# Kernel optimization log

Measured on AMD Instinct MI355X. Metric: run time of the kernel, lower is better.

Reference implementation:

```python
import jax, jax.numpy as jnp
import numpy as np

D_IN, D_HEAD, D_EXPAND, D_OUT, H = 512, 64, 2048, 512, 8
D_Q = D_HEAD * H  # 512
D_K = D_HEAD * H  # 512
D_V = D_IN * H    # 4096 (non-standard: per-head value dim = d_in)
EPS = 1e-5


def layernorm(x, g, b):
    mu = jnp.mean(x, axis=-1, keepdims=True)
    var = jnp.mean(jnp.square(x - mu), axis=-1, keepdims=True)
    return (x - mu) * jax.lax.rsqrt(var + EPS) * g + b


def setup_inputs() -> dict:
    key = jax.random.key(0)
    ks = jax.random.split(key, 12)
    B, N = 2, 2048
    s_in = 1.0 / np.sqrt(D_IN)
    s_mh = 1.0 / np.sqrt(D_IN * H)
    s_ex = 1.0 / np.sqrt(D_EXPAND)
    return {
        "x": jax.random.normal(ks[0], (B, N, D_IN), jnp.float32),
        "ln1_g": jnp.ones((D_IN,), jnp.float32),
        "ln1_b": jnp.zeros((D_IN,), jnp.float32),
        "Wqkv": jax.random.normal(ks[1], (D_IN, D_Q + D_K + D_V), jnp.float32) * s_in,
        "bqkv": jax.random.normal(ks[2], (D_Q + D_K + D_V,), jnp.float32) * 0.01,
        "Wm": jax.random.normal(ks[3], (D_IN * H, D_IN), jnp.float32) * s_mh,
        "bm": jax.random.normal(ks[4], (D_IN,), jnp.float32) * 0.01,
        "ln2_g": jnp.ones((D_IN,), jnp.float32),
        "ln2_b": jnp.zeros((D_IN,), jnp.float32),
        "W1": jax.random.normal(ks[5], (D_IN, D_EXPAND), jnp.float32) * s_in,
        "b1": jax.random.normal(ks[6], (D_EXPAND,), jnp.float32) * 0.01,
        "W2": jax.random.normal(ks[7], (D_EXPAND, D_OUT), jnp.float32) * s_ex,
        "b2": jax.random.normal(ks[8], (D_OUT,), jnp.float32) * 0.01,
    }


def reference(x, ln1_g, ln1_b, Wqkv, bqkv, Wm, bm, ln2_g, ln2_b, W1, b1, W2, b2):
    B, N, _ = x.shape
    scale = D_HEAD ** -0.5
    qkv = layernorm(x, ln1_g, ln1_b) @ Wqkv + bqkv
    q, k, v = jnp.split(qkv, [D_Q, D_Q + D_K], axis=-1)
    q = q.reshape(B, N, H, D_HEAD).transpose(0, 2, 1, 3)  # (B,H,N,dh)
    k = k.reshape(B, N, H, D_HEAD).transpose(0, 2, 1, 3)
    v = v.reshape(B, N, H, D_IN).transpose(0, 2, 1, 3)    # (B,H,N,d_in)
    attn = jax.nn.softmax(jnp.einsum('bhnd,bhmd->bhnm', q, k) * scale, axis=-1)
    out = jnp.einsum('bhnm,bhmc->bhnc', attn, v)          # (B,H,N,d_in)
    out = out.transpose(0, 2, 1, 3).reshape(B, N, H * D_IN)
    x2 = x + out @ Wm + bm
    h = layernorm(x2, ln2_g, ln2_b) @ W1 + b1
    h = h * jax.nn.sigmoid(h)  # Swish
    return h @ W2 + b2 + x2    # shortcut = Identity (d_in == d_out)
```

## Files before the change

kernel.cpp:

```cpp
#include <hip/hip_runtime.h>
#include <cmath>

typedef unsigned short u16;
typedef unsigned int   u32;
typedef __attribute__((ext_vector_type(8))) __bf16 bf16x8;
typedef __attribute__((ext_vector_type(4))) float  f32x4;
typedef __attribute__((ext_vector_type(8))) unsigned short u16x8;
typedef __attribute__((ext_vector_type(4))) unsigned short u16x4;

#define DEV __device__ __forceinline__

DEV float bf2f(u16 u){ union{u32 i; float f;} v; v.i=((u32)u)<<16; return v.f; }
DEV u16 f2bf(float f){ union{float f; u32 i;} v; v.f=f; u32 r=v.i+0x7fffu+((v.i>>16)&1u); return (u16)(r>>16); }

#if defined(__has_builtin) && __has_builtin(__builtin_amdgcn_global_load_lds)
DEV void gld16(const void* g, void* l){
  __builtin_amdgcn_global_load_lds((__attribute__((address_space(1))) void*)g,
                                   (__attribute__((address_space(3))) void*)l, 16, 0, 0);
}
#else
DEV void gld16(const void* g, void* l){ *(u16x8*)l = *(const u16x8*)g; }
#endif

#if defined(__has_builtin) && __has_builtin(__builtin_amdgcn_exp2f)
DEV float fexp2(float x){ return __builtin_amdgcn_exp2f(x); }
#else
DEV float fexp2(float x){ return exp2f(x); }
#endif

__global__ void detect_k(const u16* __restrict__ x, int* __restrict__ flag)
{
  if (threadIdx.x == 0 && blockIdx.x == 0){
    int sane = 0;
    for (int i = 0; i < 64; ++i){
      int e = (x[i] >> 7) & 0xFF;
      sane += (e >= 100 && e <= 150);
    }
    *flag = (sane < 56) ? 1 : 0;
  }
}

__global__ __launch_bounds__(256)
void conv_vecs(const void* a0,const void* a1,const void* a2,const void* a3,
               const void* a4,const void* a5,const void* a6,const void* a7,
               float* __restrict__ dst, const int* __restrict__ flag)
{
  int i = blockIdx.x*256 + threadIdx.x;
  if (i >= 10240) return;
  const void* src; int off;
  if      (i < 512)  { src=a0; off=i; }
  else if (i < 1024) { src=a1; off=i-512; }
  else if (i < 6144) { src=a2; off=i-1024; }
  else if (i < 6656) { src=a3; off=i-6144; }
  else if (i < 7168) { src=a4; off=i-6656; }
  else if (i < 7680) { src=a5; off=i-7168; }
  else if (i < 9728) { src=a6; off=i-7680; }
  else               { src=a7; off=i-9728; }
  dst[i] = (*flag) ? ((const float*)src)[off] : bf2f(((const u16*)src)[off]);
}

#define SWZ_SRC(c) (((c)&7) ^ (((c)>>3)&7))

template<int SWZ>
DEV void remap_xcd(int& bx, int& by)
{
  if (SWZ==1){
    int L = by*(int)gridDim.x + bx;
    int xcd = L & 7, l = L >> 3;
    int chunk = (int)gridDim.x >> 3;
    bx = xcd*chunk + (l % chunk);
    by = l / chunk;
  } else if (SWZ==2){
    int L = by*(int)gridDim.x + bx;
    int xcd = L & 7, l = L >> 3;
    int chunk = (int)gridDim.y >> 3;
    by = xcd*chunk + (l % chunk);
    bx = l / chunk;
  }
}

template<int MODE, int SWZ, bool VT>
__global__ __launch_bounds__(256)
void gemm_bt(const u16* __restrict__ A, const u16* __restrict__ BT,
             void* __restrict__ C, const float* __restrict__ bias,
             int K, int lda, int ldb, int ldc, u16* __restrict__ vout)
{
  __shared__ u16 AB[2*128*64];
  u16* As = AB;
  u16* Bs = AB + 128*64;
  const int tid  = threadIdx.x;
  const int lane = tid & 63;
  const int quad = lane>>4, l7 = lane&7, l15 = lane&15;
  const int wv   = tid >> 6;
  const int wm   = wv >> 1, wn = wv & 1;
  int bx = blockIdx.x, by = blockIdx.y;
  remap_xcd<SWZ>(bx, by);
  const long m0 = (long)by * 128;
  const long n0 = (long)bx * 128;

  f32x4 acc[4][4];
#pragma unroll
  for (int i=0;i<4;i++)
#pragma unroll
    for (int j=0;j<4;j++) acc[i][j] = (f32x4){0.f,0.f,0.f,0.f};

  for (int k0=0; k0<K; k0+=64){
    __syncthreads();
#pragma unroll
    for (int i=0;i<4;i++){
      int c = i*256 + tid;
      gld16(A  + (m0 + (c>>3))*lda + k0 + SWZ_SRC(c)*8, &As[c*8]);
      gld16(BT + (n0 + (c>>3))*ldb + k0 + SWZ_SRC(c)*8, &Bs[c*8]);
    }
    __syncthreads();
#pragma unroll
    for (int kk=0;kk<2;kk++){
      const int ch = ((kk*4 + quad) ^ l7) * 8;
      bf16x8 af[4], bfr[4];
#pragma unroll
      for (int t=0;t<4;t++){
        af[t]  = *(const bf16x8*)&As[(wm*64 + t*16 + l15)*64 + ch];
        bfr[t] = *(const bf16x8*)&Bs[(wn*64 + t*16 + l15)*64 + ch];
      }
#pragma unroll
      for (int ti=0;ti<4;ti++)
#pragma unroll
        for (int tj=0;tj<4;tj++)
          acc[ti][tj] = __builtin_amdgcn_mfma_f32_16x16x32_bf16(af[ti], bfr[tj], acc[ti][tj], 0,0,0);
    }
  }

  if (VT && n0 >= 1024){
    const int hh   = (int)((n0 - 1024) >> 9);
    const int c0   = (int)((n0 - 1024) & 511);
    const int b_   = (int)(m0 >> 11);
    const int kloc = (int)(m0 & 2047);
    u16* vb = vout + ((long)(b_*8 + hh))*512*2048 + kloc;
    u16* Ts = AB;
    __syncthreads();
#pragma unroll
    for (int pass=0; pass<2; ++pass){
      if (pass) __syncthreads();
      if (wn == pass){
#pragma unroll
        for (int ti=0;ti<4;ti++)
#pragma unroll
        for (int tj=0;tj<4;tj++)
#pragma unroll
        for (int r=0;r<4;r++){
          int row = wm*64 + ti*16 + quad*4 + r;
          int cl  = tj*16 + l15;
          float v = acc[ti][tj][r] + bias[n0 + pass*64 + cl];
          Ts[row*68 + cl] = f2bf(v);
        }
      }
      __syncthreads();
#pragma unroll
      for (int step=0; step<4; ++step){
        int cr = step*16 + (tid>>4);
        int t8 = (tid&15)*8;
        u16x8 pk;
#pragma unroll
        for (int j=0;j<8;j++) pk[j] = Ts[(t8+j)*68 + cr];
        *(u16x8*)(vb + (long)(c0 + pass*64 + cr)*2048 + t8) = pk;
      }
    }
    return;
  }

#pragma unroll
  for (int ti=0;ti<4;ti++)
#pragma unroll
  for (int tj=0;tj<4;tj++)
#pragma unroll
  for (int r=0;r<4;r++){
    long row = m0 + wm*64 + ti*16 + quad*4 + r;
    long col = n0 + wn*64 + tj*16 + l15;
    float v = acc[ti][tj][r] + bias[col];
    if (MODE==2) v = v / (1.f + __expf(-v));
    ((u16*)C)[row*ldc+col] = f2bf(v);
  }
}

template<int MODE, int SWZ>
__global__ __launch_bounds__(512)
void gemm_n64(const u16* __restrict__ A, const u16* __restrict__ BT,
              void* __restrict__ C, const float* __restrict__ bias,
              const void* __restrict__ res,
              int K, int lda, int ldb, int ldc, const int* __restrict__ flag)
{
  __shared__ u16 As[2][128*64];
  __shared__ u16 Bs[2][64*64];
  const int tid  = threadIdx.x;
  const int lane = tid & 63;
  const int quad = lane>>4, l7 = lane&7, l15 = lane&15;
  const int wm   = tid >> 6;
  int bx = blockIdx.x, by = blockIdx.y;
  remap_xcd<SWZ>(bx, by);
  const long m0 = (long)by * 128;
  const long n0 = (long)bx * 64;
  const bool f32io = flag && (*flag != 0);

  f32x4 acc[4];
#pragma unroll
  for (int j=0;j<4;j++) acc[j] = (f32x4){0.f,0.f,0.f,0.f};

  auto stage = [&](int bi, int k0){
#pragma unroll
    for (int i=0;i<2;i++){
      int c = i*512 + tid;
      gld16(A + (m0 + (c>>3))*lda + k0 + SWZ_SRC(c)*8, &As[bi][c*8]);
    }
    { int c = tid;
      gld16(BT + (n0 + (c>>3))*ldb + k0 + SWZ_SRC(c)*8, &Bs[bi][c*8]); }
  };

  const int S = K >> 6;
  stage(0, 0);
  __syncthreads();

  for (int s=0; s<S; ++s){
    const int cb = s & 1;
    if (s+1 < S) stage(cb^1, (s+1)<<6);
#pragma unroll
    for (int kk=0;kk<2;kk++){
      const int ch = ((kk*4 + quad) ^ l7) * 8;
      bf16x8 af = *(const bf16x8*)&As[cb][(wm*16 + l15)*64 + ch];
      bf16x8 bfr[4];
#pragma unroll
      for (int t=0;t<4;t++)
        bfr[t] = *(const bf16x8*)&Bs[cb][(t*16 + l15)*64 + ch];
#pragma unroll
      for (int tj=0;tj<4;tj++)
        acc[tj] = __builtin_amdgcn_mfma_f32_16x16x32_bf16(af, bfr[tj], acc[tj], 0,0,0);
    }
    __syncthreads();
  }

#pragma unroll
  for (int tj=0;tj<4;tj++)
#pragma unroll
  for (int r=0;r<4;r++){
    long row = m0 + wm*16 + quad*4 + r;
    long col = n0 + tj*16 + l15;
    float v = acc[tj][r] + bias[col];
    if (MODE==1){
      v += f32io ? ((const float*)res)[row*ldc+col]
                 : bf2f(((const u16*)res)[row*ldc+col]);
      ((float*)C)[row*ldc+col] = v;
    } else {
      v += ((const float*)res)[row*ldc+col];
      if (f32io) ((float*)C)[row*ldc+col] = v;
      else       ((u16*)C)[row*ldc+col]   = f2bf(v);
    }
  }
}

__global__ __launch_bounds__(512, 2)
void att_flash(const u16* __restrict__ qkv, const u16* __restrict__ vt,
               u16* __restrict__ ao)
{
  __shared__ u16 Qs[128*64];
  __shared__ u16 Ks[2][64*64];
  __shared__ u16 Ps[128*68];
  __shared__ u16 Vs[512*64];
  __shared__ float m_run[128], l_run[128], alph[128];
  __shared__ int resc[2];
  const int tid=threadIdx.x, lane=tid&63, wv=tid>>6;
  const int wm=wv>>2, wn=wv&3;
  const int quad=lane>>4, l7=lane&7, l15=lane&15;
  const int bid = blockIdx.x;
  const int id  = ((bid&7)<<5) + (bid>>3);
  const int qt  = id & 15, bh = id >> 4;
  const int b = bh>>3, h = bh&7;
  const long q0 = (long)qt*128;
  const u16* qb = qkv + ((long)b*2048 + q0)*5120 + h*64;
  const u16* kb = qkv + (long)b*2048*5120 + 512 + h*64;
  const u16* vb = vt + (long)bh*512*2048;

#pragma unroll
  for (int i=0;i<2;i++){
    int c=i*512+tid;
    gld16(qb + (long)(c>>3)*5120 + SWZ_SRC(c)*8, &Qs[c*8]);
  }
  { int c=tid; gld16(kb + (long)(c>>3)*5120 + SWZ_SRC(c)*8, &Ks[0][c*8]); }
  if (tid<128){ m_run[tid] = -1e30f; l_run[tid] = 0.f; }
  if (tid==0){ resc[0]=0; resc[1]=0; }

  f32x4 o[4][8];
#pragma unroll
  for (int i=0;i<4;i++)
#pragma unroll
    for (int j=0;j<8;j++) o[i][j] = (f32x4){0.f,0.f,0.f,0.f};

  __syncthreads();
  bf16x8 qreg[2];
#pragma unroll
  for (int kk=0;kk<2;kk++)
    qreg[kk] = *(const bf16x8*)&Qs[(wv*16 + l15)*64 + ((kk*4 + quad) ^ l7)*8];

  for (int mt=0; mt<32; ++mt){
    const long m0 = (long)mt*64;
    const int cur = mt&1;
    __syncthreads();

    if (mt < 31){ int c=tid; gld16(kb + (m0+64 + (c>>3))*5120 + SWZ_SRC(c)*8, &Ks[cur^1][c*8]); }
#pragma unroll
    for (int i=0;i<8;i++){
      int c=i*512+tid;
      gld16(vb + (long)(c>>3)*2048 + m0 + SWZ_SRC(c)*8, &Vs[c*8]);
    }
    if (tid==0) resc[cur^1] = 0;

    f32x4 s[4];
#pragma unroll
    for (int j=0;j<4;j++) s[j] = (f32x4){0.f,0.f,0.f,0.f};
#pragma unroll
    for (int kk=0;kk<2;kk++){
      const int ch = ((kk*4 + quad) ^ l7) * 8;
#pragma unroll
      for (int tj=0;tj<4;tj++){
        bf16x8 bfr = *(const bf16x8*)&Ks[cur][(tj*16 + l15)*64 + ch];
        s[tj] = __builtin_amdgcn_mfma_f32_16x16x32_bf16(qreg[kk], bfr, s[tj], 0,0,0);
      }
    }

    float nm[4], al[4], rs[4];
    bool chg = false;
#pragma unroll
    for (int r=0;r<4;r++){
      float vm = fmaxf(fmaxf(s[0][r],s[1][r]), fmaxf(s[2][r],s[3][r]));
      vm = fmaxf(vm, __shfl_xor(vm,1)); vm = fmaxf(vm, __shfl_xor(vm,2));
      vm = fmaxf(vm, __shfl_xor(vm,4)); vm = fmaxf(vm, __shfl_xor(vm,8));
      float mo = m_run[wv*16 + quad*4 + r];
      float vs = vm*0.125f;
      bool c_ = (vs > mo + 8.f);
      nm[r] = c_ ? vs : mo;
      al[r] = c_ ? __expf(mo - vs) : 1.f;
      chg |= c_;
      rs[r] = 0.f;
    }
    float nml[4];
#pragma unroll
    for (int r=0;r<4;r++) nml[r] = nm[r]*1.44269504f;
#pragma unroll
    for (int tj=0;tj<4;tj++)
#pragma unroll
    for (int r=0;r<4;r++){
      float pv = fexp2(fmaf(s[tj][r], 0.18033688f, -nml[r]));
      rs[r] += pv;
      Ps[(wv*16 + quad*4 + r)*68 + tj*16 + l15] = f2bf(pv);
    }
#pragma unroll
    for (int r=0;r<4;r++){
      rs[r] += __shfl_xor(rs[r],1); rs[r] += __shfl_xor(rs[r],2);
      rs[r] += __shfl_xor(rs[r],4); rs[r] += __shfl_xor(rs[r],8);
    }
    if (l15==0){
#pragma unroll
      for (int r=0;r<4;r++){
        int row = wv*16 + quad*4 + r;
        alph[row]  = al[r];
        m_run[row] = nm[r];
        l_run[row] = l_run[row]*al[r] + rs[r];
      }
    }
    if (__any((int)chg) && lane==0) resc[cur] = 1;
    __syncthreads();

    if (resc[cur]){
      float a_[4][4];
#pragma unroll
      for (int ti=0;ti<4;ti++)
#pragma unroll
        for (int r=0;r<4;r++) a_[ti][r] = alph[wm*64 + ti*16 + quad*4 + r];
#pragma unroll
      for (int ti=0;ti<4;ti++)
#pragma unroll
      for (int tj=0;tj<8;tj++)
#pragma unroll
        for (int r=0;r<4;r++) o[ti][tj][r] *= a_[ti][r];
    }
#pragma unroll
    for (int kk=0;kk<2;kk++){
      const int ch = ((kk*4 + quad) ^ l7) * 8;
      bf16x8 af[4], bfr[8];
#pragma unroll
      for (int t=0;t<4;t++){
        int base = (wm*64 + t*16 + l15)*68 + kk*32 + quad*8;
        union { u16x4 hh[2]; bf16x8 v; } u;
        u.hh[0] = *(const u16x4*)&Ps[base];
        u.hh[1] = *(const u16x4*)&Ps[base+4];
        af[t] = u.v;
      }
#pragma unroll
      for (int t=0;t<8;t++)
        bfr[t] = *(const bf16x8*)&Vs[(wn*128 + t*16 + l15)*64 + ch];
#pragma unroll
      for (int ti=0;ti<4;ti++)
#pragma unroll
        for (int tj=0;tj<8;tj++)
          o[ti][tj] = __builtin_amdgcn_mfma_f32_16x16x32_bf16(af[ti], bfr[tj], o[ti][tj], 0,0,0);
    }
  }

  float rl[4][4];
#pragma unroll
  for (int ti=0;ti<4;ti++)
#pragma unroll
    for (int r=0;r<4;r++) rl[ti][r] = 1.f / l_run[wm*64 + ti*16 + quad*4 + r];
#pragma unroll
  for (int ti=0;ti<4;ti++)
#pragma unroll
  for (int tj=0;tj<8;tj++)
#pragma unroll
  for (int r=0;r<4;r++){
    long rown = q0 + wm*64 + ti*16 + quad*4 + r;
    long col  = wn*128 + tj*16 + l15;
    ao[((long)b*2048 + rown)*4096 + (long)h*512 + col] = f2bf(o[ti][tj][r]*rl[ti][r]);
  }
}

template<int SRC>
__global__ __launch_bounds__(256)
void ln_kernel(const void* __restrict__ xin, const float* __restrict__ g,
               const float* __restrict__ bb, u16* __restrict__ out,
               const int* __restrict__ flag)
{
  const int tid=threadIdx.x, lane=tid&63, wv=tid>>6;
  const long row = (long)blockIdx.x*4 + wv;
  const bool f32 = (SRC==1) || (flag && *flag != 0);
  float v[8];
  if (f32){
    const float* xr = (const float*)xin + row*512 + lane*8;
#pragma unroll
    for (int j=0;j<8;j++) v[j]=xr[j];
  } else {
    const u16* xr = (const u16*)xin + row*512 + lane*8;
    u16x8 xv = *(const u16x8*)xr;
#pragma unroll
    for (int j=0;j<8;j++) v[j]=bf2f(xv[j]);
  }
  float s1=0.f, s2=0.f;
#pragma unroll
  for (int j=0;j<8;j++){ s1+=v[j]; s2+=v[j]*v[j]; }
  for (int off=1; off<64; off<<=1){ s1+=__shfl_xor(s1,off); s2+=__shfl_xor(s2,off); }
  float mu  = s1*(1.f/512.f);
  float var = s2*(1.f/512.f) - mu*mu;
  float rs  = rsqrtf(var + 1e-5f);
  u16x8 ov;
#pragma unroll
  for (int j=0;j<8;j++){
    int col = lane*8+j;
    ov[j] = f2bf((v[j]-mu)*rs*g[col] + bb[col]);
  }
  *(u16x8*)(out + row*512 + lane*8) = ov;
}

template<bool DUAL>
__global__ __launch_bounds__(256)
void transpose_k(const void* __restrict__ in_, u16* __restrict__ out,
                 int ldi, int ldo, long izh, long izl, long oz,
                 const int* __restrict__ flag)
{
  __shared__ u16 t[32][33];
  const int z = blockIdx.z;
  const bool f32 = DUAL && flag && (*flag != 0);
  const long zoff = (long)(z>>3)*izh + (long)(z&7)*izl;
  out += (long)z*oz;
  const int tx = threadIdx.x, ty = threadIdx.y;
  const long c  = (long)blockIdx.x*32 + tx;
  const long r0 = (long)blockIdx.y*32;
  if (f32){
    const float* in = (const float*)in_ + zoff;
#pragma unroll
    for (int j=0;j<4;j++) t[ty+j*8][tx] = f2bf(in[(r0+ty+j*8)*ldi + c]);
  } else {
    const u16* in = (const u16*)in_ + zoff;
#pragma unroll
    for (int j=0;j<4;j++) t[ty+j*8][tx] = in[(r0+ty+j*8)*ldi + c];
  }
  __syncthreads();
  const long rr = r0 + tx;
  const long cc = (long)blockIdx.x*32 + ty;
#pragma unroll
  for (int j=0;j<4;j++) out[(cc+j*8)*ldo + rr] = t[tx][ty+j*8];
}

extern "C" void kernel_launch(void* const* d_in, const int* in_sizes, int n_in,
                              void* d_out, int out_size, void* d_ws, size_t ws_size,
                              hipStream_t stream)
{
  const void* x    = d_in[0];
  const void* ln1g = d_in[1];
  const void* ln1b = d_in[2];
  const void* Wqkv = d_in[3];
  const void* bqkv = d_in[4];
  const void* Wm   = d_in[5];
  const void* bm   = d_in[6];
  const void* ln2g = d_in[7];
  const void* ln2b = d_in[8];
  const void* W1   = d_in[9];
  const void* b1   = d_in[10];
  const void* W2   = d_in[11];
  const void* b2   = d_in[12];

  char* p = (char*)d_ws;
  auto take = [&](size_t n){ void* r=(void*)p; p += (n + 255) & ~(size_t)255; return r; };
  u16*   lnb   = (u16*)  take((size_t)4096*512*2);
  u16*   qkv   = (u16*)  take((size_t)4096*5120*2);
  u16*   vtb   = (u16*)  take((size_t)16*512*2048*2);
  u16*   wqkvT = (u16*)  take((size_t)5120*512*2);
  u16*   wmT   = (u16*)  take((size_t)512*4096*2);
  u16*   w1T   = (u16*)  take((size_t)2048*512*2);
  u16*   w2T   = (u16*)  take((size_t)512*2048*2);
  u16*   ao    = (u16*)  take((size_t)4096*4096*2);
  float* cvec  = (float*)take((size_t)10240*4);
  int*   flag  = (int*)  take(4);
  float* x2    = (float*)vtb;
  u16*   hb    = qkv;

  detect_k<<<1, 64, 0, stream>>>((const u16*)x, flag);
  conv_vecs<<<40, 256, 0, stream>>>(ln1g, ln1b, bqkv, bm, ln2g, ln2b, b1, b2, cvec, flag);

  dim3 tb(32,8);
  transpose_k<true><<<dim3(160,16,1), tb, 0, stream>>>(Wqkv, wqkvT, 5120, 512, 0,0,0, flag);
  transpose_k<true><<<dim3(16,128,1), tb, 0, stream>>>(Wm,   wmT,   512, 4096, 0,0,0, flag);
  transpose_k<true><<<dim3(64,16,1),  tb, 0, stream>>>(W1,   w1T,  2048, 512, 0,0,0, flag);
  transpose_k<true><<<dim3(16,64,1),  tb, 0, stream>>>(W2,   w2T,   512, 2048, 0,0,0, flag);

  ln_kernel<0><<<1024, 256, 0, stream>>>(x, cvec+0, cvec+512, lnb, flag);
  gemm_bt<0,1,true><<<dim3(40,32), 256, 0, stream>>>(lnb, wqkvT, qkv, cvec+1024,
                                                     512, 512, 512, 5120, vtb);

  att_flash<<<dim3(256), 512, 0, stream>>>(qkv, vtb, ao);

  gemm_n64<1,2><<<dim3(8,32), 512, 0, stream>>>(ao, wmT, x2, cvec+6144, x,
                                                4096, 4096, 4096, 512, flag);
  ln_kernel<1><<<1024, 256, 0, stream>>>(x2, cvec+6656, cvec+7168, lnb, nullptr);
  gemm_bt<2,2,false><<<dim3(16,32), 256, 0, stream>>>(lnb, w1T, hb, cvec+7680,
                                                      512, 512, 512, 2048, nullptr);
  gemm_n64<3,2><<<dim3(8,32), 512, 0, stream>>>(hb, w2T, d_out, cvec+9728, x2,
                                                2048, 2048, 2048, 512, flag);
}
```

Measured before the change: 378.6 us.

## Double-buffer gemm_bt LDS tiles and use 8 waves per 128x128 block

The gemm_bt kernel moves from 4 to 8 waves per block. Each wave now computes a 64x32 sub-tile instead of 64x64. The K loop becomes double-buffered: the next K-slice is staged into a second LDS buffer while MFMAs run on the current one, which removes one barrier per iteration. The V-transpose epilogue is simplified into a single pass over a 128x132 LDS tile. LDS use doubles to 64KB per block, which may lower occupancy, and each wave has fewer MFMAs per LDS fragment load.

```diff
diff --git a/kernel.cpp b/kernel.cpp
--- a/kernel.cpp
+++ b/kernel.cpp
@@ -80,54 +80,63 @@
 }
 
 template<int MODE, int SWZ, bool VT>
-__global__ __launch_bounds__(256)
+__global__ __launch_bounds__(512)
 void gemm_bt(const u16* __restrict__ A, const u16* __restrict__ BT,
              void* __restrict__ C, const float* __restrict__ bias,
              int K, int lda, int ldb, int ldc, u16* __restrict__ vout)
 {
-  __shared__ u16 AB[2*128*64];
-  u16* As = AB;
-  u16* Bs = AB + 128*64;
+  __shared__ u16 AB[4*128*64];
+  u16* As0 = AB;
+  u16* Bs0 = AB + 2*128*64;
   const int tid  = threadIdx.x;
   const int lane = tid & 63;
   const int quad = lane>>4, l7 = lane&7, l15 = lane&15;
   const int wv   = tid >> 6;
-  const int wm   = wv >> 1, wn = wv & 1;
+  const int wm   = wv >> 2, wn = wv & 3;
   int bx = blockIdx.x, by = blockIdx.y;
   remap_xcd<SWZ>(bx, by);
   const long m0 = (long)by * 128;
   const long n0 = (long)bx * 128;
 
-  f32x4 acc[4][4];
+  f32x4 acc[4][2];
 #pragma unroll
   for (int i=0;i<4;i++)
 #pragma unroll
-    for (int j=0;j<4;j++) acc[i][j] = (f32x4){0.f,0.f,0.f,0.f};
-
-  for (int k0=0; k0<K; k0+=64){
-    __syncthreads();
-#pragma unroll
-    for (int i=0;i<4;i++){
-      int c = i*256 + tid;
-      gld16(A  + (m0 + (c>>3))*lda + k0 + SWZ_SRC(c)*8, &As[c*8]);
-      gld16(BT + (n0 + (c>>3))*ldb + k0 + SWZ_SRC(c)*8, &Bs[c*8]);
-    }
-    __syncthreads();
+    for (int j=0;j<2;j++) acc[i][j] = (f32x4){0.f,0.f,0.f,0.f};
+
+  auto stage = [&](int bi, int k0){
+#pragma unroll
+    for (int i=0;i<2;i++){
+      int c = i*512 + tid;
+      gld16(A  + (m0 + (c>>3))*lda + k0 + SWZ_SRC(c)*8, &As0[bi*8192 + c*8]);
+      gld16(BT + (n0 + (c>>3))*ldb + k0 + SWZ_SRC(c)*8, &Bs0[bi*8192 + c*8]);
+    }
+  };
+
+  const int S = K >> 6;
+  stage(0, 0);
+  __syncthreads();
+
+  for (int s=0; s<S; ++s){
+    const int cb = s & 1;
+    if (s+1 < S) stage(cb^1, (s+1)<<6);
 #pragma unroll
     for (int kk=0;kk<2;kk++){
       const int ch = ((kk*4 + quad) ^ l7) * 8;
-      bf16x8 af[4], bfr[4];
-#pragma unroll
-      for (int t=0;t<4;t++){
-        af[t]  = *(const bf16x8*)&As[(wm*64 + t*16 + l15)*64 + ch];
-        bfr[t] = *(const bf16x8*)&Bs[(wn*64 + t*16 + l15)*64 + ch];
-      }
+      bf16x8 af[4], bfr[2];
+#pragma unroll
+      for (int t=0;t<4;t++)
+        af[t]  = *(const bf16x8*)&As0[cb*8192 + (wm*64 + t*16 + l15)*64 + ch];
+#pragma unroll
+      for (int t=0;t<2;t++)
+        bfr[t] = *(const bf16x8*)&Bs0[cb*8192 + (wn*32 + t*16 + l15)*64 + ch];
 #pragma unroll
       for (int ti=0;ti<4;ti++)
 #pragma unroll
-        for (int tj=0;tj<4;tj++)
+        for (int tj=0;tj<2;tj++)
           acc[ti][tj] = __builtin_amdgcn_mfma_f32_16x16x32_bf16(af[ti], bfr[tj], acc[ti][tj], 0,0,0);
     }
+    __syncthreads();
   }
 
   if (VT && n0 >= 1024){
@@ -137,33 +146,25 @@
     const int kloc = (int)(m0 & 2047);
     u16* vb = vout + ((long)(b_*8 + hh))*512*2048 + kloc;
     u16* Ts = AB;
+#pragma unroll
+    for (int ti=0;ti<4;ti++)
+#pragma unroll
+    for (int tj=0;tj<2;tj++)
+#pragma unroll
+    for (int r=0;r<4;r++){
+      int row = wm*64 + ti*16 + quad*4 + r;
+      int cl  = wn*32 + tj*16 + l15;
+      Ts[row*132 + cl] = f2bf(acc[ti][tj][r] + bias[n0 + cl]);
+    }
     __syncthreads();
 #pragma unroll
-    for (int pass=0; pass<2; ++pass){
-      if (pass) __syncthreads();
-      if (wn == pass){
-#pragma unroll
-        for (int ti=0;ti<4;ti++)
-#pragma unroll
-        for (int tj=0;tj<4;tj++)
-#pragma unroll
-        for (int r=0;r<4;r++){
-          int row = wm*64 + ti*16 + quad*4 + r;
-          int cl  = tj*16 + l15;
-          float v = acc[ti][tj][r] + bias[n0 + pass*64 + cl];
-          Ts[row*68 + cl] = f2bf(v);
-        }
-      }
-      __syncthreads();
-#pragma unroll
-      for (int step=0; step<4; ++step){
-        int cr = step*16 + (tid>>4);
-        int t8 = (tid&15)*8;
-        u16x8 pk;
-#pragma unroll
-        for (int j=0;j<8;j++) pk[j] = Ts[(t8+j)*68 + cr];
-        *(u16x8*)(vb + (long)(c0 + pass*64 + cr)*2048 + t8) = pk;
-      }
+    for (int step=0; step<4; ++step){
+      int cr = step*32 + (tid>>4);
+      int t8 = (tid&15)*8;
+      u16x8 pk;
+#pragma unroll
+      for (int j=0;j<8;j++) pk[j] = Ts[(t8+j)*132 + cr];
+      *(u16x8*)(vb + (long)(c0 + cr)*2048 + t8) = pk;
     }
     return;
   }
@@ -171,11 +172,11 @@
 #pragma unroll
   for (int ti=0;ti<4;ti++)
 #pragma unroll
-  for (int tj=0;tj<4;tj++)
+  for (int tj=0;tj<2;tj++)
 #pragma unroll
   for (int r=0;r<4;r++){
     long row = m0 + wm*64 + ti*16 + quad*4 + r;
-    long col = n0 + wn*64 + tj*16 + l15;
+    long col = n0 + wn*32 + tj*16 + l15;
     float v = acc[ti][tj][r] + bias[col];
     if (MODE==2) v = v / (1.f + __expf(-v));
     ((u16*)C)[row*ldc+col] = f2bf(v);
@@ -530,7 +531,7 @@
   transpose_k<true><<<dim3(16,64,1),  tb, 0, stream>>>(W2,   w2T,   512, 2048, 0,0,0, flag);
 
   ln_kernel<0><<<1024, 256, 0, stream>>>(x, cvec+0, cvec+512, lnb, flag);
-  gemm_bt<0,1,true><<<dim3(40,32), 256, 0, stream>>>(lnb, wqkvT, qkv, cvec+1024,
+  gemm_bt<0,1,true><<<dim3(40,32), 512, 0, stream>>>(lnb, wqkvT, qkv, cvec+1024,
                                                      512, 512, 512, 5120, vtb);
 
   att_flash<<<dim3(256), 512, 0, stream>>>(qkv, vtb, ao);
@@ -538,7 +539,7 @@
   gemm_n64<1,2><<<dim3(8,32), 512, 0, stream>>>(ao, wmT, x2, cvec+6144, x,
                                                 4096, 4096, 4096, 512, flag);
   ln_kernel<1><<<1024, 256, 0, stream>>>(x2, cvec+6656, cvec+7168, lnb, nullptr);
-  gemm_bt<2,2,false><<<dim3(16,32), 256, 0, stream>>>(lnb, w1T, hb, cvec+7680,
+  gemm_bt<2,2,false><<<dim3(16,32), 512, 0, stream>>>(lnb, w1T, hb, cvec+7680,
                                                       512, 512, 512, 2048, nullptr);
   gemm_n64<3,2><<<dim3(8,32), 512, 0, stream>>>(hb, w2T, d_out, cvec+9728, x2,
                                                 2048, 2048, 2048, 512, flag);
```

After: 359.1 us. -5.2%, faster.
